# Kernel optimization log

Measured on AMD Instinct MI355X. Metric: run time of the kernel, lower is better.

Reference implementation:

```python
import jax, jax.numpy as jnp
import numpy as np

N_NODES, N_EDGES = 50000, 200000
OUT, IN_SELF, EDGE_DIM = 32, 128, 16


def setup_inputs() -> dict:
    key = jax.random.key(0)
    ks = jax.random.split(key, 9)
    return {
        "h_neigh": jax.random.normal(ks[0], (N_NODES, OUT), jnp.float32),
        "h_self": jax.random.normal(ks[1], (N_NODES, IN_SELF), jnp.float32),
        "edge_features": jax.random.normal(ks[2], (N_EDGES, EDGE_DIM), jnp.float32),
        "W_edge": jax.random.normal(ks[3], (OUT * OUT, EDGE_DIM), jnp.float32) * 0.05,
        "b_edge": jax.random.normal(ks[4], (OUT * OUT,), jnp.float32) * 0.05,
        "W_self": jax.random.normal(ks[5], (OUT, IN_SELF), jnp.float32) * 0.05,
        "W_neigh": jax.random.normal(ks[6], (OUT, OUT), jnp.float32) * 0.05,
        "src": jax.random.randint(ks[7], (N_EDGES,), 0, N_NODES),
        "dst": jax.random.randint(ks[8], (N_EDGES,), 0, N_NODES),
    }


def reference(h_neigh, h_self, edge_features, W_edge, b_edge, W_self, W_neigh, src, dst):
    E = edge_features.shape[0]
    N = h_neigh.shape[0]
    out = W_self.shape[0]
    # per-edge weight matrices: [E, out, out]
    ew = (edge_features @ W_edge.T + b_edge).reshape(E, out, out)
    # u_mul_e: m[e,i,j] = h_src[e,j] * ew[e,i,j]; downstream does mean over edges
    # then sum over i. Sum over i commutes with mean, so fuse: s[e,j] =
    # h_src[e,j] * sum_i ew[e,i,j]  -> identical math, [E,out] messages.
    s = h_neigh[src] * ew.sum(axis=1)  # [E, out]
    deg = jax.ops.segment_sum(jnp.ones((E,), s.dtype), dst, num_segments=N)
    agg = jax.ops.segment_sum(s, dst, num_segments=N) / jnp.maximum(deg, 1.0)[:, None]
    z = jax.nn.relu(h_self @ W_self.T + agg @ W_neigh.T)
    return z
```

## Files before the change

kernel.cpp:

```cpp
#include <hip/hip_runtime.h>

#define N_NODES 50000
#define N_EDGES 200000
#define OUT 32
#define IN_SELF 128
#define EDGE_DIM 16

__global__ void prep_kernel(const float* __restrict__ W_edge,
                            const float* __restrict__ b_edge,
                            float* __restrict__ Wcol, float* __restrict__ bcol) {
    int t = threadIdx.x;
    if (t < OUT * EDGE_DIM) {
        int j = t / EDGE_DIM, k = t % EDGE_DIM;
        float s = 0.f;
#pragma unroll
        for (int i = 0; i < OUT; ++i) s += W_edge[(i * OUT + j) * EDGE_DIM + k];
        Wcol[t] = s;
    }
    if (t < OUT) {
        float s = 0.f;
#pragma unroll
        for (int i = 0; i < OUT; ++i) s += b_edge[i * OUT + t];
        bcol[t] = s;
    }
}

__global__ void edge_kernel(const float* __restrict__ h_neigh,
                            const float* __restrict__ ef,
                            const int* __restrict__ src,
                            const int* __restrict__ dst,
                            const float* __restrict__ Wcol,
                            const float* __restrict__ bcol,
                            float* __restrict__ agg,
                            float* __restrict__ deg, int E) {
    __shared__ float wl[OUT][EDGE_DIM + 1];
    __shared__ float bl[OUT];
    __shared__ float efl[8][EDGE_DIM];
    int t = threadIdx.x;
    for (int i = t; i < OUT * EDGE_DIM; i += 256)
        wl[i / EDGE_DIM][i % EDGE_DIM] = Wcol[i];
    if (t < OUT) bl[t] = bcol[t];
    int e0 = blockIdx.x * 8;
    if (t < 8 * EDGE_DIM) {
        int e = e0 + t / EDGE_DIM;
        if (e < E) efl[t / EDGE_DIM][t % EDGE_DIM] = ef[e * EDGE_DIM + t % EDGE_DIM];
    }
    __syncthreads();

    int le = t >> 5, j = t & 31;
    int e = e0 + le;
    if (e >= E) return;
    int s = src[e];
    int d = dst[e];
    float acc = bl[j];
#pragma unroll
    for (int k = 0; k < EDGE_DIM; ++k) acc += efl[le][k] * wl[j][k];
    float hv = h_neigh[s * OUT + j];
    atomicAdd(&agg[d * OUT + j], hv * acc);
    if (j == 0) atomicAdd(&deg[d], 1.0f);
}

__global__ void node_kernel(const float* __restrict__ h_self,
                            const float* __restrict__ agg,
                            const float* __restrict__ deg,
                            const float* __restrict__ W_self,
                            const float* __restrict__ W_neigh,
                            float* __restrict__ out, int N) {
    __shared__ float ws[OUT][IN_SELF + 1];
    __shared__ float wn[OUT][OUT + 1];
    __shared__ float hs[8][IN_SELF];
    __shared__ float an[8][OUT];
    int t = threadIdx.x;
    for (int i = t; i < OUT * IN_SELF; i += 256) ws[i >> 7][i & 127] = W_self[i];
    for (int i = t; i < OUT * OUT; i += 256) wn[i >> 5][i & 31] = W_neigh[i];
    int n0 = blockIdx.x * 8;
    for (int i = t; i < 8 * IN_SELF; i += 256) {
        int n = n0 + (i >> 7);
        if (n < N) hs[i >> 7][i & 127] = h_self[n * IN_SELF + (i & 127)];
    }
    {
        int n = n0 + (t >> 5);
        if (n < N) {
            float dg = fmaxf(deg[n], 1.0f);
            an[t >> 5][t & 31] = agg[n * OUT + (t & 31)] / dg;
        }
    }
    __syncthreads();

    int ln = t >> 5, j = t & 31;
    int n = n0 + ln;
    if (n >= N) return;
    float acc = 0.f;
#pragma unroll 8
    for (int k = 0; k < IN_SELF; ++k) acc += hs[ln][k] * ws[j][k];
#pragma unroll
    for (int k = 0; k < OUT; ++k) acc += an[ln][k] * wn[j][k];
    out[n * OUT + j] = fmaxf(acc, 0.f);
}

extern "C" void kernel_launch(void* const* d_in, const int* in_sizes, int n_in,
                              void* d_out, int out_size, void* d_ws, size_t ws_size,
                              hipStream_t stream) {
    const float* h_neigh = (const float*)d_in[0];
    const float* h_self  = (const float*)d_in[1];
    const float* ef      = (const float*)d_in[2];
    const float* W_edge  = (const float*)d_in[3];
    const float* b_edge  = (const float*)d_in[4];
    const float* W_self  = (const float*)d_in[5];
    const float* W_neigh = (const float*)d_in[6];
    const int*   src     = (const int*)d_in[7];
    const int*   dst     = (const int*)d_in[8];
    float* out = (float*)d_out;

    const int N = N_NODES, E = N_EDGES;

    float* Wcol = (float*)d_ws;
    float* bcol = Wcol + OUT * EDGE_DIM;
    float* deg  = bcol + OUT;
    float* agg  = deg + N;

    hipMemsetAsync(deg, 0, (size_t)(N + N * OUT) * sizeof(float), stream);

    prep_kernel<<<1, 512, 0, stream>>>(W_edge, b_edge, Wcol, bcol);

    edge_kernel<<<(E + 7) / 8, 256, 0, stream>>>(h_neigh, ef, src, dst, Wcol, bcol,
                                                 agg, deg, E);

    node_kernel<<<(N + 7) / 8, 256, 0, stream>>>(h_self, agg, deg, W_self, W_neigh,
                                                 out, N);
}
```

Before: 169.7 us.

## Fuse memset into prep kernel, batch edges per block, vectorize shared loads

```diff
diff --git a/kernel.cpp b/kernel.cpp
--- a/kernel.cpp
+++ b/kernel.cpp
@@ -6,83 +6,113 @@
 #define IN_SELF 128
 #define EDGE_DIM 16
 
-__global__ void prep_kernel(const float* __restrict__ W_edge,
-                            const float* __restrict__ b_edge,
-                            float* __restrict__ Wcol, float* __restrict__ bcol) {
-    int t = threadIdx.x;
-    if (t < OUT * EDGE_DIM) {
-        int j = t / EDGE_DIM, k = t % EDGE_DIM;
-        float s = 0.f;
+__global__ __launch_bounds__(256) void prep_zero_kernel(
+        const float* __restrict__ W_edge, const float* __restrict__ b_edge,
+        float* __restrict__ Wcol, float* __restrict__ bcol,
+        float4* __restrict__ zero4, int n_zero4) {
+    int gid = blockIdx.x * 256 + threadIdx.x;
+    for (int i = gid; i < n_zero4; i += gridDim.x * 256) {
+        zero4[i] = make_float4(0.f, 0.f, 0.f, 0.f);
+    }
+    if (blockIdx.x == 0) {
+        int t = threadIdx.x;
+        for (int i = t; i < OUT * EDGE_DIM; i += 256) {
+            int j = i / EDGE_DIM, k = i % EDGE_DIM;
+            float s = 0.f;
 #pragma unroll
-        for (int i = 0; i < OUT; ++i) s += W_edge[(i * OUT + j) * EDGE_DIM + k];
-        Wcol[t] = s;
-    }
-    if (t < OUT) {
-        float s = 0.f;
+            for (int r = 0; r < OUT; ++r) s += W_edge[(r * OUT + j) * EDGE_DIM + k];
+            Wcol[i] = s;
+        }
+        if (t < OUT) {
+            float s = 0.f;
 #pragma unroll
-        for (int i = 0; i < OUT; ++i) s += b_edge[i * OUT + t];
-        bcol[t] = s;
+            for (int r = 0; r < OUT; ++r) s += b_edge[r * OUT + t];
+            bcol[t] = s;
+        }
     }
 }
 
-__global__ void edge_kernel(const float* __restrict__ h_neigh,
-                            const float* __restrict__ ef,
-                            const int* __restrict__ src,
-                            const int* __restrict__ dst,
-                            const float* __restrict__ Wcol,
-                            const float* __restrict__ bcol,
-                            float* __restrict__ agg,
-                            float* __restrict__ deg, int E) {
-    __shared__ float wl[OUT][EDGE_DIM + 1];
+__global__ __launch_bounds__(256) void edge_kernel(
+        const float* __restrict__ h_neigh, const float* __restrict__ ef,
+        const int* __restrict__ src, const int* __restrict__ dst,
+        const float* __restrict__ Wcol, const float* __restrict__ bcol,
+        float* __restrict__ agg, float* __restrict__ deg, int E) {
+    __shared__ float4 wl4[OUT][5];
+    __shared__ float4 efl[32][4];
     __shared__ float bl[OUT];
-    __shared__ float efl[8][EDGE_DIM];
+    __shared__ int sdl[32], ddl[32];
+
     int t = threadIdx.x;
-    for (int i = t; i < OUT * EDGE_DIM; i += 256)
-        wl[i / EDGE_DIM][i % EDGE_DIM] = Wcol[i];
-    if (t < OUT) bl[t] = bcol[t];
-    int e0 = blockIdx.x * 8;
-    if (t < 8 * EDGE_DIM) {
-        int e = e0 + t / EDGE_DIM;
-        if (e < E) efl[t / EDGE_DIM][t % EDGE_DIM] = ef[e * EDGE_DIM + t % EDGE_DIM];
+    int e0 = blockIdx.x * 32;
+    if (t < 128) {
+        wl4[t >> 2][t & 3] = ((const float4*)Wcol)[t];
+    } else {
+        int i = t - 128;
+        int e = e0 + (i >> 2);
+        if (e < E) efl[i >> 2][i & 3] = ((const float4*)ef)[(size_t)e * 4 + (i & 3)];
+    }
+    if (t < 32) {
+        bl[t] = bcol[t];
+        sdl[t] = (e0 + t < E) ? src[e0 + t] : 0;
+    } else if (t < 64) {
+        int i = t - 32;
+        ddl[i] = (e0 + i < E) ? dst[e0 + i] : 0;
     }
     __syncthreads();
 
-    int le = t >> 5, j = t & 31;
-    int e = e0 + le;
-    if (e >= E) return;
-    int s = src[e];
-    int d = dst[e];
-    float acc = bl[j];
+    int g = t >> 5, j = t & 31;
 #pragma unroll
-    for (int k = 0; k < EDGE_DIM; ++k) acc += efl[le][k] * wl[j][k];
-    float hv = h_neigh[s * OUT + j];
-    atomicAdd(&agg[d * OUT + j], hv * acc);
-    if (j == 0) atomicAdd(&deg[d], 1.0f);
+    for (int it = 0; it < 4; ++it) {
+        int le = g + 8 * it;
+        int e = e0 + le;
+        if (e >= E) continue;
+        int s = sdl[le];
+        int d = ddl[le];
+        float4 w0 = wl4[j][0], w1 = wl4[j][1], w2 = wl4[j][2], w3 = wl4[j][3];
+        float4 f0 = efl[le][0], f1 = efl[le][1], f2 = efl[le][2], f3 = efl[le][3];
+        float acc = bl[j];
+        acc = fmaf(f0.x, w0.x, acc); acc = fmaf(f0.y, w0.y, acc);
+        acc = fmaf(f0.z, w0.z, acc); acc = fmaf(f0.w, w0.w, acc);
+        acc = fmaf(f1.x, w1.x, acc); acc = fmaf(f1.y, w1.y, acc);
+        acc = fmaf(f1.z, w1.z, acc); acc = fmaf(f1.w, w1.w, acc);
+        acc = fmaf(f2.x, w2.x, acc); acc = fmaf(f2.y, w2.y, acc);
+        acc = fmaf(f2.z, w2.z, acc); acc = fmaf(f2.w, w2.w, acc);
+        acc = fmaf(f3.x, w3.x, acc); acc = fmaf(f3.y, w3.y, acc);
+        acc = fmaf(f3.z, w3.z, acc); acc = fmaf(f3.w, w3.w, acc);
+        float hv = h_neigh[(size_t)s * OUT + j];
+        atomicAdd(&agg[(size_t)d * OUT + j], hv * acc);
+        if (j == 0) atomicAdd(&deg[d], 1.0f);
+    }
 }
 
-__global__ void node_kernel(const float* __restrict__ h_self,
-                            const float* __restrict__ agg,
-                            const float* __restrict__ deg,
-                            const float* __restrict__ W_self,
-                            const float* __restrict__ W_neigh,
-                            float* __restrict__ out, int N) {
-    __shared__ float ws[OUT][IN_SELF + 1];
-    __shared__ float wn[OUT][OUT + 1];
-    __shared__ float hs[8][IN_SELF];
-    __shared__ float an[8][OUT];
+__global__ __launch_bounds__(256) void node_kernel(
+        const float* __restrict__ h_self, const float* __restrict__ agg,
+        const float* __restrict__ deg, const float* __restrict__ W_self,
+        const float* __restrict__ W_neigh, float* __restrict__ out, int N) {
+    __shared__ float4 ws4[OUT][33];
+    __shared__ float4 wn4[OUT][9];
+    __shared__ float4 hs4[8][32];
+    __shared__ float4 an4[8][8];
+
     int t = threadIdx.x;
-    for (int i = t; i < OUT * IN_SELF; i += 256) ws[i >> 7][i & 127] = W_self[i];
-    for (int i = t; i < OUT * OUT; i += 256) wn[i >> 5][i & 31] = W_neigh[i];
     int n0 = blockIdx.x * 8;
-    for (int i = t; i < 8 * IN_SELF; i += 256) {
-        int n = n0 + (i >> 7);
-        if (n < N) hs[i >> 7][i & 127] = h_self[n * IN_SELF + (i & 127)];
+
+    for (int i = t; i < OUT * (IN_SELF / 4); i += 256)
+        ws4[i >> 5][i & 31] = ((const float4*)W_self)[i];
+    {
+        wn4[t >> 3][t & 7] = ((const float4*)W_neigh)[t];
     }
     {
         int n = n0 + (t >> 5);
+        if (n < N) hs4[t >> 5][t & 31] = ((const float4*)h_self)[(size_t)n0 * 32 + t];
+    }
+    if (t < 64) {
+        int ln = t >> 3, k4 = t & 7;
+        int n = n0 + ln;
         if (n < N) {
-            float dg = fmaxf(deg[n], 1.0f);
-            an[t >> 5][t & 31] = agg[n * OUT + (t & 31)] / dg;
+            float r = 1.0f / fmaxf(deg[n], 1.0f);
+            float4 v = ((const float4*)agg)[(size_t)n * 8 + k4];
+            an4[ln][k4] = make_float4(v.x * r, v.y * r, v.z * r, v.w * r);
         }
     }
     __syncthreads();
@@ -90,12 +120,21 @@
     int ln = t >> 5, j = t & 31;
     int n = n0 + ln;
     if (n >= N) return;
-    float acc = 0.f;
-#pragma unroll 8
-    for (int k = 0; k < IN_SELF; ++k) acc += hs[ln][k] * ws[j][k];
+    float4 a4 = make_float4(0.f, 0.f, 0.f, 0.f);
 #pragma unroll
-    for (int k = 0; k < OUT; ++k) acc += an[ln][k] * wn[j][k];
-    out[n * OUT + j] = fmaxf(acc, 0.f);
+    for (int k4 = 0; k4 < IN_SELF / 4; ++k4) {
+        float4 h = hs4[ln][k4], w = ws4[j][k4];
+        a4.x = fmaf(h.x, w.x, a4.x); a4.y = fmaf(h.y, w.y, a4.y);
+        a4.z = fmaf(h.z, w.z, a4.z); a4.w = fmaf(h.w, w.w, a4.w);
+    }
+#pragma unroll
+    for (int k4 = 0; k4 < OUT / 4; ++k4) {
+        float4 h = an4[ln][k4], w = wn4[j][k4];
+        a4.x = fmaf(h.x, w.x, a4.x); a4.y = fmaf(h.y, w.y, a4.y);
+        a4.z = fmaf(h.z, w.z, a4.z); a4.w = fmaf(h.w, w.w, a4.w);
+    }
+    float acc = (a4.x + a4.y) + (a4.z + a4.w);
+    out[(size_t)n * OUT + j] = fmaxf(acc, 0.f);
 }
 
 extern "C" void kernel_launch(void* const* d_in, const int* in_sizes, int n_in,
@@ -119,13 +158,15 @@
     float* deg  = bcol + OUT;
     float* agg  = deg + N;
 
-    hipMemsetAsync(deg, 0, (size_t)(N + N * OUT) * sizeof(float), stream);
+    const int n_zero4 = (N + N * OUT) / 4;
+    const int zgrid = (n_zero4 + 255) / 256;
 
-    prep_kernel<<<1, 512, 0, stream>>>(W_edge, b_edge, Wcol, bcol);
+    prep_zero_kernel<<<zgrid, 256, 0, stream>>>(W_edge, b_edge, Wcol, bcol,
+                                                (float4*)deg, n_zero4);
 
-    edge_kernel<<<(E + 7) / 8, 256, 0, stream>>>(h_neigh, ef, src, dst, Wcol, bcol,
-                                                 agg, deg, E);
+    edge_kernel<<<(E + 31) / 32, 256, 0, stream>>>(h_neigh, ef, src, dst,
+                                                   Wcol, bcol, agg, deg, E);
 
-    node_kernel<<<(N + 7) / 8, 256, 0, stream>>>(h_self, agg, deg, W_self, W_neigh,
-                                                 out, N);
+    node_kernel<<<(N + 7) / 8, 256, 0, stream>>>(h_self, agg, deg, W_self,
+                                                 W_neigh, out, N);
 }
```

Result: faster. 150.8 us (-11.2%).
